# Optimization experiments

Hardware: AMD Instinct MI355X
Metric: run time of the kernel (lower is better)

Reference implementation:

```python
import jax, jax.numpy as jnp
import numpy as np

ROBOT_ACT, DIRECTION, RESOURCE, REPEAT = 6, 5, 5, 2
EMB, Q = 64, 20
NEG_SLOPE = 0.01  # nn.LeakyReLU default


def setup_inputs() -> dict:
    key = jax.random.key(0)
    ks = jax.random.split(key, 16)
    B, H, W = 16, 48, 48
    inp = {
        "unit_indicator": jax.random.randint(ks[0], (B, H, W), 0, 2).astype(bool),
        "act_type": jax.random.randint(ks[1], (B, H, W, Q), 0, ROBOT_ACT).astype(jnp.int32),
        "direction": jax.random.randint(ks[2], (B, H, W, Q), 0, DIRECTION).astype(jnp.int32),
        "resource": jax.random.randint(ks[3], (B, H, W, Q), 0, RESOURCE).astype(jnp.int32),
        "repeat": jax.random.randint(ks[4], (B, H, W, Q), 0, REPEAT).astype(jnp.int32),
        "amount": jax.random.uniform(ks[5], (B, H, W, Q), jnp.float32),
        "n": jax.random.uniform(ks[6], (B, H, W, Q), jnp.float32),
        # learned params
        "type_table": jax.random.normal(ks[7], (ROBOT_ACT, EMB), jnp.float32),
        "direction_table": jax.random.normal(ks[8], (DIRECTION, EMB), jnp.float32),
        "resource_table": jax.random.normal(ks[9], (RESOURCE, EMB), jnp.float32),
        "repeat_table": jax.random.normal(ks[10], (REPEAT, EMB), jnp.float32),
        "w1": jax.random.normal(ks[11], (Q,), jnp.float32) / np.sqrt(Q),   # Conv3d(1,1,(Q,1,1)) weight
        "b1": jax.random.normal(ks[12], (1,), jnp.float32) * 0.1,
        "w2": jax.random.normal(ks[13], (6,), jnp.float32) / np.sqrt(6.0),  # Conv3d(1,1,(1,1,6)) weight
        "b2": jax.random.normal(ks[14], (1,), jnp.float32) * 0.1,
    }
    return inp


def reference(unit_indicator, act_type, direction, resource, repeat, amount, n,
              type_table, direction_table, resource_table, repeat_table,
              w1, b1, w2, b2):
    # Stack order along the size-6 conv axis: [type, direction, resource, amount, repeat, n].
    # Both conv3ds are linear, so out = LeakyReLU(sum_f w2[f] * (sum_q w1[q]*feat[q,f]) + b1*sum(w2) + b2).
    rep_idx = (repeat != 0).astype(jnp.int32)
    # Per-table: gather [B,H,W,Q,E], contract Q with w1 -> [B,H,W,E]
    c = (w2[0] * jnp.einsum('q,bhwqe->bhwe', w1, type_table[act_type])
         + w2[1] * jnp.einsum('q,bhwqe->bhwe', w1, direction_table[direction])
         + w2[2] * jnp.einsum('q,bhwqe->bhwe', w1, resource_table[resource])
         + w2[4] * jnp.einsum('q,bhwqe->bhwe', w1, repeat_table[rep_idx])
         + (w2[3] * jnp.einsum('q,bhwq->bhw', w1, amount))[..., None]
         + (w2[5] * jnp.einsum('q,bhwq->bhw', w1, n))[..., None]
         + b1 * jnp.sum(w2) + b2)
    out = jnp.where(c >= 0, c, NEG_SLOPE * c)
    out = out * unit_indicator[..., None].astype(out.dtype)  # zeros where no unit
    return jnp.transpose(out, (0, 3, 1, 2))  # [B, E, H, W]
```

## Files before the change

kernel.cpp:

```cpp
#include <hip/hip_runtime.h>

constexpr int Q    = 20;
constexpr int EMB  = 64;
constexpr int Bsz  = 16, H = 48, W = 48;
constexpr int HW   = H * W;
constexpr int NPIX = Bsz * HW;
constexpr int BLOCK = 128;
constexpr int TPP   = 4;
constexpr int PIXPB = BLOCK / TPP;
constexpr int NBLK  = NPIX / PIXPB;

__global__ __launch_bounds__(BLOCK)
void act_pre_kernel(const int* __restrict__ unit,
                    const int* __restrict__ atp,  const int* __restrict__ dirp,
                    const int* __restrict__ resp, const int* __restrict__ repp,
                    const float* __restrict__ amtp, const float* __restrict__ np_,
                    const float* __restrict__ Ttab, const float* __restrict__ Dtab,
                    const float* __restrict__ Rtab, const float* __restrict__ Ptab,
                    const float* __restrict__ w1p,  const float* __restrict__ b1p,
                    const float* __restrict__ w2p,  const float* __restrict__ b2p,
                    float* __restrict__ out)
{
    __shared__ float sc[15][EMB];

    const int tid = threadIdx.x;
    const int pIB = tid >> 2;
    const int t   = tid & 3;
    const int pix = blockIdx.x * PIXPB + pIB;

    const int base = pix * Q + t * 4;
    const int4   av = *reinterpret_cast<const int4*>(atp  + base);
    const int4   dv = *reinterpret_cast<const int4*>(dirp + base);
    const int4   rv = *reinterpret_cast<const int4*>(resp + base);
    const int4   pv = *reinterpret_cast<const int4*>(repp + base);
    const float4 mv = *reinterpret_cast<const float4*>(amtp + base);
    const float4 nv = *reinterpret_cast<const float4*>(np_  + base);
    const int tail  = pix * Q + 16 + t;
    const int   as = atp[tail],  ds2 = dirp[tail], rs = resp[tail], ps = repp[tail];
    const float ms = amtp[tail], ns = np_[tail];
    const int   uu = unit[pix];
    const float4 wv = *reinterpret_cast<const float4*>(w1p + t * 4);
    const float  ws = w1p[16 + t];

    const float w20 = w2p[0], w21 = w2p[1], w22 = w2p[2];
    const float w23 = w2p[3], w24 = w2p[4], w25 = w2p[5];
    const float constC = b1p[0] * (w20 + w21 + w22 + w23 + w24 + w25) + b2p[0];

    for (int i = tid; i < 15 * EMB; i += BLOCK) {
        const int row = i >> 6, e = i & 63;
        float v;
        if (row < 5)        v = w20 * (Ttab[row * EMB + e]       - Ttab[5 * EMB + e]);
        else if (row < 9)   v = w21 * (Dtab[(row - 5) * EMB + e] - Dtab[4 * EMB + e]);
        else if (row < 13)  v = w22 * (Rtab[(row - 9) * EMB + e] - Rtab[4 * EMB + e]);
        else if (row == 13) v = w24 * (Ptab[EMB + e] - Ptab[e]);
        else {
            float sumw = 0.f;
            #pragma unroll
            for (int q = 0; q < Q; ++q) sumw += w1p[q];
            v = sumw * (w20 * Ttab[5 * EMB + e] + w21 * Dtab[4 * EMB + e]
                      + w22 * Rtab[4 * EMB + e] + w24 * Ptab[e]);
        }
        sc[row][e] = v;
    }

    const int   ai[5] = {av.x, av.y, av.z, av.w, as};
    const int   di[5] = {dv.x, dv.y, dv.z, dv.w, ds2};
    const int   ri[5] = {rv.x, rv.y, rv.z, rv.w, rs};
    const int   pi[5] = {pv.x, pv.y, pv.z, pv.w, ps};
    const float mf[5] = {mv.x, mv.y, mv.z, mv.w, ms};
    const float nf[5] = {nv.x, nv.y, nv.z, nv.w, ns};
    const float wf[5] = {wv.x, wv.y, wv.z, wv.w, ws};

    float cT[5] = {}, cD[4] = {}, cR[4] = {};
    float rep = 0.f, amtAcc = 0.f, nAcc = 0.f;
    #pragma unroll
    for (int j = 0; j < 5; ++j) {
        const float wq = wf[j];
        #pragma unroll
        for (int k = 0; k < 5; ++k) cT[k] += (ai[j] == k) ? wq : 0.f;
        #pragma unroll
        for (int k = 0; k < 4; ++k) cD[k] += (di[j] == k) ? wq : 0.f;
        #pragma unroll
        for (int k = 0; k < 4; ++k) cR[k] += (ri[j] == k) ? wq : 0.f;
        rep    += (pi[j] != 0) ? wq : 0.f;
        amtAcc += wq * mf[j];
        nAcc   += wq * nf[j];
    }

    #define RED4(x) { x += __shfl_xor(x, 1); x += __shfl_xor(x, 2); }
    #pragma unroll
    for (int k = 0; k < 5; ++k) RED4(cT[k]);
    #pragma unroll
    for (int k = 0; k < 4; ++k) RED4(cD[k]);
    #pragma unroll
    for (int k = 0; k < 4; ++k) RED4(cR[k]);
    RED4(rep); RED4(amtAcc); RED4(nAcc);
    #undef RED4

    const float scalar = w23 * amtAcc + w25 * nAcc + constC;
    const float ind = (uu != 0) ? 1.f : 0.f;

    float coef[14];
    #pragma unroll
    for (int k = 0; k < 5; ++k) coef[k] = cT[k];
    #pragma unroll
    for (int k = 0; k < 4; ++k) coef[5 + k] = cD[k];
    #pragma unroll
    for (int k = 0; k < 4; ++k) coef[9 + k] = cR[k];
    coef[13] = rep;

    const int b  = pix / HW;
    const int hw = pix - b * HW;
    float* outp = out + b * (EMB * HW) + hw;

    __syncthreads();

    #pragma unroll
    for (int i = 0; i < 4; ++i) {
        const int e0 = t * 16 + i * 4;
        const float4 bv = *reinterpret_cast<const float4*>(&sc[14][e0]);
        float va0 = scalar + bv.x, va1 = scalar + bv.y;
        float va2 = scalar + bv.z, va3 = scalar + bv.w;
        #pragma unroll
        for (int k = 0; k < 14; ++k) {
            const float4 sv = *reinterpret_cast<const float4*>(&sc[k][e0]);
            va0 += coef[k] * sv.x;
            va1 += coef[k] * sv.y;
            va2 += coef[k] * sv.z;
            va3 += coef[k] * sv.w;
        }
        va0 = ((va0 >= 0.f) ? va0 : 0.01f * va0) * ind;
        va1 = ((va1 >= 0.f) ? va1 : 0.01f * va1) * ind;
        va2 = ((va2 >= 0.f) ? va2 : 0.01f * va2) * ind;
        va3 = ((va3 >= 0.f) ? va3 : 0.01f * va3) * ind;
        outp[(e0 + 0) * HW] = va0;
        outp[(e0 + 1) * HW] = va1;
        outp[(e0 + 2) * HW] = va2;
        outp[(e0 + 3) * HW] = va3;
    }
}

extern "C" void kernel_launch(void* const* d_in, const int* in_sizes, int n_in,
                              void* d_out, int out_size, void* d_ws, size_t ws_size,
                              hipStream_t stream) {
    const int*   unit = (const int*)  d_in[0];
    const int*   atp  = (const int*)  d_in[1];
    const int*   dirp = (const int*)  d_in[2];
    const int*   resp = (const int*)  d_in[3];
    const int*   repp = (const int*)  d_in[4];
    const float* amtp = (const float*)d_in[5];
    const float* np_  = (const float*)d_in[6];
    const float* Ttab = (const float*)d_in[7];
    const float* Dtab = (const float*)d_in[8];
    const float* Rtab = (const float*)d_in[9];
    const float* Ptab = (const float*)d_in[10];
    const float* w1p  = (const float*)d_in[11];
    const float* b1p  = (const float*)d_in[12];
    const float* w2p  = (const float*)d_in[13];
    const float* b2p  = (const float*)d_in[14];
    float* out = (float*)d_out;

    act_pre_kernel<<<NBLK, BLOCK, 0, stream>>>(
        unit, atp, dirp, resp, repp, amtp, np_,
        Ttab, Dtab, Rtab, Ptab, w1p, b1p, w2p, b2p, out);
}
```

Measured before the change: 14.20 us.

## Process two pixels per thread and compute bias row from reduced w1 sum

Each thread now handles two pixels, 32 apart, so a block covers 64 pixels and the per-block shared table setup is amortized over twice the work, halving the block count. The bias row no longer loops over all 20 w1 values per element: w1 is partially summed per lane and shuffle-reduced, and the row is written after the coefficient reductions. The table-build loop is fully unrolled to 7 iterations. This raises register pressure and halves grid parallelism, and relies on 64 pixels per block never crossing a batch boundary, which holds since HW is divisible by 64.

```diff
diff --git a/kernel.cpp b/kernel.cpp
--- a/kernel.cpp
+++ b/kernel.cpp
@@ -7,7 +7,8 @@
 constexpr int NPIX = Bsz * HW;
 constexpr int BLOCK = 128;
 constexpr int TPP   = 4;
-constexpr int PIXPB = BLOCK / TPP;
+constexpr int PXPT  = 2;
+constexpr int PIXPB = BLOCK / TPP * PXPT;
 constexpr int NBLK  = NPIX / PIXPB;
 
 __global__ __launch_bounds__(BLOCK)
@@ -23,95 +24,133 @@
 {
     __shared__ float sc[15][EMB];
 
-    const int tid = threadIdx.x;
-    const int pIB = tid >> 2;
-    const int t   = tid & 3;
-    const int pix = blockIdx.x * PIXPB + pIB;
-
-    const int base = pix * Q + t * 4;
-    const int4   av = *reinterpret_cast<const int4*>(atp  + base);
-    const int4   dv = *reinterpret_cast<const int4*>(dirp + base);
-    const int4   rv = *reinterpret_cast<const int4*>(resp + base);
-    const int4   pv = *reinterpret_cast<const int4*>(repp + base);
-    const float4 mv = *reinterpret_cast<const float4*>(amtp + base);
-    const float4 nv = *reinterpret_cast<const float4*>(np_  + base);
-    const int tail  = pix * Q + 16 + t;
-    const int   as = atp[tail],  ds2 = dirp[tail], rs = resp[tail], ps = repp[tail];
-    const float ms = amtp[tail], ns = np_[tail];
-    const int   uu = unit[pix];
+    const int tid  = threadIdx.x;
+    const int pIB  = tid >> 2;
+    const int t    = tid & 3;
+    const int pixA = blockIdx.x * PIXPB + pIB;
+    const int pixB = pixA + 32;
+
+    const int baseA = pixA * Q + t * 4, tailA = pixA * Q + 16 + t;
+    const int baseB = pixB * Q + t * 4, tailB = pixB * Q + 16 + t;
+    const int4   avA = *reinterpret_cast<const int4*>(atp  + baseA);
+    const int4   dvA = *reinterpret_cast<const int4*>(dirp + baseA);
+    const int4   rvA = *reinterpret_cast<const int4*>(resp + baseA);
+    const int4   pvA = *reinterpret_cast<const int4*>(repp + baseA);
+    const float4 mvA = *reinterpret_cast<const float4*>(amtp + baseA);
+    const float4 nvA = *reinterpret_cast<const float4*>(np_  + baseA);
+    const int4   avB = *reinterpret_cast<const int4*>(atp  + baseB);
+    const int4   dvB = *reinterpret_cast<const int4*>(dirp + baseB);
+    const int4   rvB = *reinterpret_cast<const int4*>(resp + baseB);
+    const int4   pvB = *reinterpret_cast<const int4*>(repp + baseB);
+    const float4 mvB = *reinterpret_cast<const float4*>(amtp + baseB);
+    const float4 nvB = *reinterpret_cast<const float4*>(np_  + baseB);
+    const int   asA = atp[tailA], dsA = dirp[tailA], rsA = resp[tailA], psA = repp[tailA];
+    const float msA = amtp[tailA], nsA = np_[tailA];
+    const int   asB = atp[tailB], dsB = dirp[tailB], rsB = resp[tailB], psB = repp[tailB];
+    const float msB = amtp[tailB], nsB = np_[tailB];
+    const int   uuA = unit[pixA], uuB = unit[pixB];
     const float4 wv = *reinterpret_cast<const float4*>(w1p + t * 4);
     const float  ws = w1p[16 + t];
+
+    float tv5 = 0.f, dv4 = 0.f, rv4 = 0.f, pv0 = 0.f;
+    if (tid < EMB) {
+        tv5 = Ttab[5 * EMB + tid];
+        dv4 = Dtab[4 * EMB + tid];
+        rv4 = Rtab[4 * EMB + tid];
+        pv0 = Ptab[tid];
+    }
 
     const float w20 = w2p[0], w21 = w2p[1], w22 = w2p[2];
     const float w23 = w2p[3], w24 = w2p[4], w25 = w2p[5];
     const float constC = b1p[0] * (w20 + w21 + w22 + w23 + w24 + w25) + b2p[0];
 
-    for (int i = tid; i < 15 * EMB; i += BLOCK) {
+    #pragma unroll
+    for (int it = 0; it < 7; ++it) {
+        const int i = it * BLOCK + tid;
         const int row = i >> 6, e = i & 63;
         float v;
-        if (row < 5)        v = w20 * (Ttab[row * EMB + e]       - Ttab[5 * EMB + e]);
-        else if (row < 9)   v = w21 * (Dtab[(row - 5) * EMB + e] - Dtab[4 * EMB + e]);
-        else if (row < 13)  v = w22 * (Rtab[(row - 9) * EMB + e] - Rtab[4 * EMB + e]);
-        else if (row == 13) v = w24 * (Ptab[EMB + e] - Ptab[e]);
-        else {
-            float sumw = 0.f;
+        if (row < 5)       v = w20 * (Ttab[row * EMB + e]       - Ttab[5 * EMB + e]);
+        else if (row < 9)  v = w21 * (Dtab[(row - 5) * EMB + e] - Dtab[4 * EMB + e]);
+        else if (row < 13) v = w22 * (Rtab[(row - 9) * EMB + e] - Rtab[4 * EMB + e]);
+        else               v = w24 * (Ptab[EMB + e] - Ptab[e]);
+        sc[row][e] = v;
+    }
+
+    const float wf[5] = {wv.x, wv.y, wv.z, wv.w, ws};
+    float sumwT = wv.x + wv.y + wv.z + wv.w + ws;
+
+    float cTA[5] = {}, cDA[4] = {}, cRA[4] = {}, repA = 0.f, amtA = 0.f, nA = 0.f;
+    float cTB[5] = {}, cDB[4] = {}, cRB[4] = {}, repB = 0.f, amtB = 0.f, nB = 0.f;
+    {
+        const int   aiA[5] = {avA.x, avA.y, avA.z, avA.w, asA};
+        const int   diA[5] = {dvA.x, dvA.y, dvA.z, dvA.w, dsA};
+        const int   riA[5] = {rvA.x, rvA.y, rvA.z, rvA.w, rsA};
+        const int   piA[5] = {pvA.x, pvA.y, pvA.z, pvA.w, psA};
+        const float mfA[5] = {mvA.x, mvA.y, mvA.z, mvA.w, msA};
+        const float nfA[5] = {nvA.x, nvA.y, nvA.z, nvA.w, nsA};
+        const int   aiB[5] = {avB.x, avB.y, avB.z, avB.w, asB};
+        const int   diB[5] = {dvB.x, dvB.y, dvB.z, dvB.w, dsB};
+        const int   riB[5] = {rvB.x, rvB.y, rvB.z, rvB.w, rsB};
+        const int   piB[5] = {pvB.x, pvB.y, pvB.z, pvB.w, psB};
+        const float mfB[5] = {mvB.x, mvB.y, mvB.z, mvB.w, msB};
+        const float nfB[5] = {nvB.x, nvB.y, nvB.z, nvB.w, nsB};
+        #pragma unroll
+        for (int j = 0; j < 5; ++j) {
+            const float wq = wf[j];
             #pragma unroll
-            for (int q = 0; q < Q; ++q) sumw += w1p[q];
-            v = sumw * (w20 * Ttab[5 * EMB + e] + w21 * Dtab[4 * EMB + e]
-                      + w22 * Rtab[4 * EMB + e] + w24 * Ptab[e]);
+            for (int k = 0; k < 5; ++k) {
+                cTA[k] += (aiA[j] == k) ? wq : 0.f;
+                cTB[k] += (aiB[j] == k) ? wq : 0.f;
+            }
+            #pragma unroll
+            for (int k = 0; k < 4; ++k) {
+                cDA[k] += (diA[j] == k) ? wq : 0.f;
+                cDB[k] += (diB[j] == k) ? wq : 0.f;
+            }
+            #pragma unroll
+            for (int k = 0; k < 4; ++k) {
+                cRA[k] += (riA[j] == k) ? wq : 0.f;
+                cRB[k] += (riB[j] == k) ? wq : 0.f;
+            }
+            repA += (piA[j] != 0) ? wq : 0.f;
+            repB += (piB[j] != 0) ? wq : 0.f;
+            amtA += wq * mfA[j];  amtB += wq * mfB[j];
+            nA   += wq * nfA[j];  nB   += wq * nfB[j];
         }
-        sc[row][e] = v;
-    }
-
-    const int   ai[5] = {av.x, av.y, av.z, av.w, as};
-    const int   di[5] = {dv.x, dv.y, dv.z, dv.w, ds2};
-    const int   ri[5] = {rv.x, rv.y, rv.z, rv.w, rs};
-    const int   pi[5] = {pv.x, pv.y, pv.z, pv.w, ps};
-    const float mf[5] = {mv.x, mv.y, mv.z, mv.w, ms};
-    const float nf[5] = {nv.x, nv.y, nv.z, nv.w, ns};
-    const float wf[5] = {wv.x, wv.y, wv.z, wv.w, ws};
-
-    float cT[5] = {}, cD[4] = {}, cR[4] = {};
-    float rep = 0.f, amtAcc = 0.f, nAcc = 0.f;
-    #pragma unroll
-    for (int j = 0; j < 5; ++j) {
-        const float wq = wf[j];
-        #pragma unroll
-        for (int k = 0; k < 5; ++k) cT[k] += (ai[j] == k) ? wq : 0.f;
-        #pragma unroll
-        for (int k = 0; k < 4; ++k) cD[k] += (di[j] == k) ? wq : 0.f;
-        #pragma unroll
-        for (int k = 0; k < 4; ++k) cR[k] += (ri[j] == k) ? wq : 0.f;
-        rep    += (pi[j] != 0) ? wq : 0.f;
-        amtAcc += wq * mf[j];
-        nAcc   += wq * nf[j];
     }
 
     #define RED4(x) { x += __shfl_xor(x, 1); x += __shfl_xor(x, 2); }
     #pragma unroll
-    for (int k = 0; k < 5; ++k) RED4(cT[k]);
-    #pragma unroll
-    for (int k = 0; k < 4; ++k) RED4(cD[k]);
-    #pragma unroll
-    for (int k = 0; k < 4; ++k) RED4(cR[k]);
-    RED4(rep); RED4(amtAcc); RED4(nAcc);
+    for (int k = 0; k < 5; ++k) { RED4(cTA[k]); RED4(cTB[k]); }
+    #pragma unroll
+    for (int k = 0; k < 4; ++k) { RED4(cDA[k]); RED4(cDB[k]); }
+    #pragma unroll
+    for (int k = 0; k < 4; ++k) { RED4(cRA[k]); RED4(cRB[k]); }
+    RED4(repA); RED4(repB); RED4(amtA); RED4(amtB); RED4(nA); RED4(nB);
+    RED4(sumwT);
     #undef RED4
 
-    const float scalar = w23 * amtAcc + w25 * nAcc + constC;
-    const float ind = (uu != 0) ? 1.f : 0.f;
-
-    float coef[14];
-    #pragma unroll
-    for (int k = 0; k < 5; ++k) coef[k] = cT[k];
-    #pragma unroll
-    for (int k = 0; k < 4; ++k) coef[5 + k] = cD[k];
-    #pragma unroll
-    for (int k = 0; k < 4; ++k) coef[9 + k] = cR[k];
-    coef[13] = rep;
-
-    const int b  = pix / HW;
-    const int hw = pix - b * HW;
-    float* outp = out + b * (EMB * HW) + hw;
+    if (tid < EMB)
+        sc[14][tid] = sumwT * (w20 * tv5 + w21 * dv4 + w22 * rv4 + w24 * pv0);
+
+    const float scalarA = w23 * amtA + w25 * nA + constC;
+    const float scalarB = w23 * amtB + w25 * nB + constC;
+    const float indA = (uuA != 0) ? 1.f : 0.f;
+    const float indB = (uuB != 0) ? 1.f : 0.f;
+
+    float cfA[14], cfB[14];
+    #pragma unroll
+    for (int k = 0; k < 5; ++k) { cfA[k] = cTA[k]; cfB[k] = cTB[k]; }
+    #pragma unroll
+    for (int k = 0; k < 4; ++k) { cfA[5 + k] = cDA[k]; cfB[5 + k] = cDB[k]; }
+    #pragma unroll
+    for (int k = 0; k < 4; ++k) { cfA[9 + k] = cRA[k]; cfB[9 + k] = cRB[k]; }
+    cfA[13] = repA; cfB[13] = repB;
+
+    const int b  = pixA / HW;
+    const int hw = pixA - b * HW;
+    float* outpA = out + b * (EMB * HW) + hw;
+    float* outpB = outpA + 32;
 
     __syncthreads();
 
@@ -119,24 +158,28 @@
     for (int i = 0; i < 4; ++i) {
         const int e0 = t * 16 + i * 4;
         const float4 bv = *reinterpret_cast<const float4*>(&sc[14][e0]);
-        float va0 = scalar + bv.x, va1 = scalar + bv.y;
-        float va2 = scalar + bv.z, va3 = scalar + bv.w;
+        float a0 = scalarA + bv.x, a1 = scalarA + bv.y, a2 = scalarA + bv.z, a3 = scalarA + bv.w;
+        float b0 = scalarB + bv.x, b1 = scalarB + bv.y, b2 = scalarB + bv.z, b3 = scalarB + bv.w;
         #pragma unroll
         for (int k = 0; k < 14; ++k) {
             const float4 sv = *reinterpret_cast<const float4*>(&sc[k][e0]);
-            va0 += coef[k] * sv.x;
-            va1 += coef[k] * sv.y;
-            va2 += coef[k] * sv.z;
-            va3 += coef[k] * sv.w;
+            a0 += cfA[k] * sv.x;  b0 += cfB[k] * sv.x;
+            a1 += cfA[k] * sv.y;  b1 += cfB[k] * sv.y;
+            a2 += cfA[k] * sv.z;  b2 += cfB[k] * sv.z;
+            a3 += cfA[k] * sv.w;  b3 += cfB[k] * sv.w;
         }
-        va0 = ((va0 >= 0.f) ? va0 : 0.01f * va0) * ind;
-        va1 = ((va1 >= 0.f) ? va1 : 0.01f * va1) * ind;
-        va2 = ((va2 >= 0.f) ? va2 : 0.01f * va2) * ind;
-        va3 = ((va3 >= 0.f) ? va3 : 0.01f * va3) * ind;
-        outp[(e0 + 0) * HW] = va0;
-        outp[(e0 + 1) * HW] = va1;
-        outp[(e0 + 2) * HW] = va2;
-        outp[(e0 + 3) * HW] = va3;
+        a0 = ((a0 >= 0.f) ? a0 : 0.01f * a0) * indA;
+        a1 = ((a1 >= 0.f) ? a1 : 0.01f * a1) * indA;
+        a2 = ((a2 >= 0.f) ? a2 : 0.01f * a2) * indA;
+        a3 = ((a3 >= 0.f) ? a3 : 0.01f * a3) * indA;
+        b0 = ((b0 >= 0.f) ? b0 : 0.01f * b0) * indB;
+        b1 = ((b1 >= 0.f) ? b1 : 0.01f * b1) * indB;
+        b2 = ((b2 >= 0.f) ? b2 : 0.01f * b2) * indB;
+        b3 = ((b3 >= 0.f) ? b3 : 0.01f * b3) * indB;
+        outpA[(e0 + 0) * HW] = a0;  outpB[(e0 + 0) * HW] = b0;
+        outpA[(e0 + 1) * HW] = a1;  outpB[(e0 + 1) * HW] = b1;
+        outpA[(e0 + 2) * HW] = a2;  outpB[(e0 + 2) * HW] = b2;
+        outpA[(e0 + 3) * HW] = a3;  outpB[(e0 + 3) * HW] = b3;
     }
 }
 
```

Result: slower. 19.02 us (+33.9%).

## Drop shared-memory table precompute; read embedding tables directly from global cache

Applied to the files above, without the earlier changes.

Removes the per-block shared-memory precomputation of differenced, weighted embedding rows and the __syncthreads that followed it. Each thread now builds full one-hot coefficient counts, including the reference row, and multiplies them directly against float4 loads of the embedding tables, which will mostly hit in cache. Block size doubles to 256. This removes redundant per-block table work and the barrier, but adds more FMAs per output (18 rows instead of 15) and more global/L1 loads in the inner loop.

```diff
diff --git a/kernel.cpp b/kernel.cpp
--- a/kernel.cpp
+++ b/kernel.cpp
@@ -5,7 +5,7 @@
 constexpr int Bsz  = 16, H = 48, W = 48;
 constexpr int HW   = H * W;
 constexpr int NPIX = Bsz * HW;
-constexpr int BLOCK = 128;
+constexpr int BLOCK = 256;
 constexpr int TPP   = 4;
 constexpr int PIXPB = BLOCK / TPP;
 constexpr int NBLK  = NPIX / PIXPB;
@@ -21,21 +21,19 @@
                     const float* __restrict__ w2p,  const float* __restrict__ b2p,
                     float* __restrict__ out)
 {
-    __shared__ float sc[15][EMB];
-
     const int tid = threadIdx.x;
     const int pIB = tid >> 2;
     const int t   = tid & 3;
     const int pix = blockIdx.x * PIXPB + pIB;
 
     const int base = pix * Q + t * 4;
+    const int tail = pix * Q + 16 + t;
     const int4   av = *reinterpret_cast<const int4*>(atp  + base);
     const int4   dv = *reinterpret_cast<const int4*>(dirp + base);
     const int4   rv = *reinterpret_cast<const int4*>(resp + base);
     const int4   pv = *reinterpret_cast<const int4*>(repp + base);
     const float4 mv = *reinterpret_cast<const float4*>(amtp + base);
     const float4 nv = *reinterpret_cast<const float4*>(np_  + base);
-    const int tail  = pix * Q + 16 + t;
     const int   as = atp[tail],  ds2 = dirp[tail], rs = resp[tail], ps = repp[tail];
     const float ms = amtp[tail], ns = np_[tail];
     const int   uu = unit[pix];
@@ -46,23 +44,6 @@
     const float w23 = w2p[3], w24 = w2p[4], w25 = w2p[5];
     const float constC = b1p[0] * (w20 + w21 + w22 + w23 + w24 + w25) + b2p[0];
 
-    for (int i = tid; i < 15 * EMB; i += BLOCK) {
-        const int row = i >> 6, e = i & 63;
-        float v;
-        if (row < 5)        v = w20 * (Ttab[row * EMB + e]       - Ttab[5 * EMB + e]);
-        else if (row < 9)   v = w21 * (Dtab[(row - 5) * EMB + e] - Dtab[4 * EMB + e]);
-        else if (row < 13)  v = w22 * (Rtab[(row - 9) * EMB + e] - Rtab[4 * EMB + e]);
-        else if (row == 13) v = w24 * (Ptab[EMB + e] - Ptab[e]);
-        else {
-            float sumw = 0.f;
-            #pragma unroll
-            for (int q = 0; q < Q; ++q) sumw += w1p[q];
-            v = sumw * (w20 * Ttab[5 * EMB + e] + w21 * Dtab[4 * EMB + e]
-                      + w22 * Rtab[4 * EMB + e] + w24 * Ptab[e]);
-        }
-        sc[row][e] = v;
-    }
-
     const int   ai[5] = {av.x, av.y, av.z, av.w, as};
     const int   di[5] = {dv.x, dv.y, dv.z, dv.w, ds2};
     const int   ri[5] = {rv.x, rv.y, rv.z, rv.w, rs};
@@ -71,17 +52,18 @@
     const float nf[5] = {nv.x, nv.y, nv.z, nv.w, ns};
     const float wf[5] = {wv.x, wv.y, wv.z, wv.w, ws};
 
-    float cT[5] = {}, cD[4] = {}, cR[4] = {};
+    float cT[6] = {}, cD[5] = {}, cR[5] = {};
     float rep = 0.f, amtAcc = 0.f, nAcc = 0.f;
+    float sumw = wf[0] + wf[1] + wf[2] + wf[3] + wf[4];
     #pragma unroll
     for (int j = 0; j < 5; ++j) {
         const float wq = wf[j];
         #pragma unroll
-        for (int k = 0; k < 5; ++k) cT[k] += (ai[j] == k) ? wq : 0.f;
+        for (int k = 0; k < 6; ++k) cT[k] += (ai[j] == k) ? wq : 0.f;
         #pragma unroll
-        for (int k = 0; k < 4; ++k) cD[k] += (di[j] == k) ? wq : 0.f;
+        for (int k = 0; k < 5; ++k) cD[k] += (di[j] == k) ? wq : 0.f;
         #pragma unroll
-        for (int k = 0; k < 4; ++k) cR[k] += (ri[j] == k) ? wq : 0.f;
+        for (int k = 0; k < 5; ++k) cR[k] += (ri[j] == k) ? wq : 0.f;
         rep    += (pi[j] != 0) ? wq : 0.f;
         amtAcc += wq * mf[j];
         nAcc   += wq * nf[j];
@@ -89,54 +71,69 @@
 
     #define RED4(x) { x += __shfl_xor(x, 1); x += __shfl_xor(x, 2); }
     #pragma unroll
-    for (int k = 0; k < 5; ++k) RED4(cT[k]);
+    for (int k = 0; k < 6; ++k) RED4(cT[k]);
     #pragma unroll
-    for (int k = 0; k < 4; ++k) RED4(cD[k]);
+    for (int k = 0; k < 5; ++k) RED4(cD[k]);
     #pragma unroll
-    for (int k = 0; k < 4; ++k) RED4(cR[k]);
-    RED4(rep); RED4(amtAcc); RED4(nAcc);
+    for (int k = 0; k < 5; ++k) RED4(cR[k]);
+    RED4(rep); RED4(amtAcc); RED4(nAcc); RED4(sumw);
     #undef RED4
 
     const float scalar = w23 * amtAcc + w25 * nAcc + constC;
     const float ind = (uu != 0) ? 1.f : 0.f;
 
-    float coef[14];
+    float dT[6], dD[5], dR[5];
     #pragma unroll
-    for (int k = 0; k < 5; ++k) coef[k] = cT[k];
+    for (int k = 0; k < 6; ++k) dT[k] = w20 * cT[k];
     #pragma unroll
-    for (int k = 0; k < 4; ++k) coef[5 + k] = cD[k];
+    for (int k = 0; k < 5; ++k) dD[k] = w21 * cD[k];
     #pragma unroll
-    for (int k = 0; k < 4; ++k) coef[9 + k] = cR[k];
-    coef[13] = rep;
+    for (int k = 0; k < 5; ++k) dR[k] = w22 * cR[k];
+    const float dP0 = w24 * (sumw - rep);
+    const float dP1 = w24 * rep;
 
     const int b  = pix / HW;
     const int hw = pix - b * HW;
     float* outp = out + b * (EMB * HW) + hw;
 
-    __syncthreads();
-
     #pragma unroll
     for (int i = 0; i < 4; ++i) {
         const int e0 = t * 16 + i * 4;
-        const float4 bv = *reinterpret_cast<const float4*>(&sc[14][e0]);
-        float va0 = scalar + bv.x, va1 = scalar + bv.y;
-        float va2 = scalar + bv.z, va3 = scalar + bv.w;
+        float a0 = scalar, a1 = scalar, a2 = scalar, a3 = scalar;
         #pragma unroll
-        for (int k = 0; k < 14; ++k) {
-            const float4 sv = *reinterpret_cast<const float4*>(&sc[k][e0]);
-            va0 += coef[k] * sv.x;
-            va1 += coef[k] * sv.y;
-            va2 += coef[k] * sv.z;
-            va3 += coef[k] * sv.w;
+        for (int j = 0; j < 6; ++j) {
+            const float4 sv = *reinterpret_cast<const float4*>(Ttab + j * EMB + e0);
+            a0 += dT[j] * sv.x;  a1 += dT[j] * sv.y;
+            a2 += dT[j] * sv.z;  a3 += dT[j] * sv.w;
         }
-        va0 = ((va0 >= 0.f) ? va0 : 0.01f * va0) * ind;
-        va1 = ((va1 >= 0.f) ? va1 : 0.01f * va1) * ind;
-        va2 = ((va2 >= 0.f) ? va2 : 0.01f * va2) * ind;
-        va3 = ((va3 >= 0.f) ? va3 : 0.01f * va3) * ind;
-        outp[(e0 + 0) * HW] = va0;
-        outp[(e0 + 1) * HW] = va1;
-        outp[(e0 + 2) * HW] = va2;
-        outp[(e0 + 3) * HW] = va3;
+        #pragma unroll
+        for (int j = 0; j < 5; ++j) {
+            const float4 sv = *reinterpret_cast<const float4*>(Dtab + j * EMB + e0);
+            a0 += dD[j] * sv.x;  a1 += dD[j] * sv.y;
+            a2 += dD[j] * sv.z;  a3 += dD[j] * sv.w;
+        }
+        #pragma unroll
+        for (int j = 0; j < 5; ++j) {
+            const float4 sv = *reinterpret_cast<const float4*>(Rtab + j * EMB + e0);
+            a0 += dR[j] * sv.x;  a1 += dR[j] * sv.y;
+            a2 += dR[j] * sv.z;  a3 += dR[j] * sv.w;
+        }
+        {
+            const float4 p0 = *reinterpret_cast<const float4*>(Ptab + e0);
+            const float4 p1 = *reinterpret_cast<const float4*>(Ptab + EMB + e0);
+            a0 += dP0 * p0.x + dP1 * p1.x;
+            a1 += dP0 * p0.y + dP1 * p1.y;
+            a2 += dP0 * p0.z + dP1 * p1.z;
+            a3 += dP0 * p0.w + dP1 * p1.w;
+        }
+        a0 = ((a0 >= 0.f) ? a0 : 0.01f * a0) * ind;
+        a1 = ((a1 >= 0.f) ? a1 : 0.01f * a1) * ind;
+        a2 = ((a2 >= 0.f) ? a2 : 0.01f * a2) * ind;
+        a3 = ((a3 >= 0.f) ? a3 : 0.01f * a3) * ind;
+        outp[(e0 + 0) * HW] = a0;
+        outp[(e0 + 1) * HW] = a1;
+        outp[(e0 + 2) * HW] = a2;
+        outp[(e0 + 3) * HW] = a3;
     }
 }
 
```

New measurement: 20.57 us. +44.9%, slower.
